# Optimization experiments

Measured on AMD Instinct MI355X. Metric: run time of the kernel, lower is better.

Reference implementation:

```python
import jax, jax.numpy as jnp
import numpy as np

MAX_LEN = 4096
HEAD_DIM = 128
NUM_HEAD = 32
NUM_KV_GROUPS = 8
NUM_HEAD_KV = NUM_HEAD // NUM_KV_GROUPS
BASE = 10000.0


def _rope_tables(seq_len):
    pos = jnp.arange(seq_len, dtype=jnp.float32)
    freq = BASE ** (-(jnp.arange(0, HEAD_DIM, 2, dtype=jnp.float32) / HEAD_DIM))
    ang = pos[:, None] * freq[None, :]  # [n, d/2]
    return jnp.cos(ang), jnp.sin(ang)


def _apply_rope(x, cos, sin):
    # x: [..., n, d]; interleaved even/odd rotation as in the torch RoPe
    even = x[..., ::2]
    odd = x[..., 1::2]
    even_r = even * cos - odd * sin
    odd_r = odd * cos + even * sin
    return jnp.stack([even_r, odd_r], axis=-1).reshape(x.shape)


def setup_inputs() -> dict:
    key = jax.random.key(0)
    ks = jax.random.split(key, 9)
    B, N, D = 4, 1024, NUM_HEAD * HEAD_DIM
    KV = NUM_HEAD_KV * HEAD_DIM
    s = 0.02
    return {
        "x": jax.random.normal(ks[0], (B, N, D), jnp.float32),
        "Wq": jax.random.normal(ks[1], (D, D), jnp.float32) * s,
        "bq": jax.random.normal(ks[2], (D,), jnp.float32) * s,
        "Wk": jax.random.normal(ks[3], (D, KV), jnp.float32) * s,
        "bk": jax.random.normal(ks[4], (KV,), jnp.float32) * s,
        "Wv": jax.random.normal(ks[5], (D, KV), jnp.float32) * s,
        "bv": jax.random.normal(ks[6], (KV,), jnp.float32) * s,
        "Wo": jax.random.normal(ks[7], (D, D), jnp.float32) * s,
        "bo": jax.random.normal(ks[8], (D,), jnp.float32) * s,
    }


def reference(x, Wq, bq, Wk, bk, Wv, bv, Wo, bo):
    B, N, _ = x.shape
    g, h, d = NUM_KV_GROUPS, NUM_HEAD_KV, HEAD_DIM
    scale = d ** (-0.5)

    q = x @ Wq + bq                      # [B, N, g*h*d]
    k = x @ Wk + bk                      # [B, N, h*d]
    v = x @ Wv + bv

    # b n (g h d) -> b g h n d (group-major, matching einops pattern)
    q = q.reshape(B, N, g, h, d).transpose(0, 2, 3, 1, 4)
    k = k.reshape(B, N, h, d).transpose(0, 2, 1, 3)   # b h n d
    v = v.reshape(B, N, h, d).transpose(0, 2, 1, 3)

    cos, sin = _rope_tables(N)
    q = _apply_rope(q, cos, sin)
    k = _apply_rope(k, cos, sin)

    attn = jnp.einsum('bghid,bhjd->bghij', q * scale, k)
    causal = jnp.tril(jnp.ones((N, N), dtype=bool))
    attn = jnp.where(causal, attn, -jnp.inf)
    attn = jax.nn.softmax(attn, axis=-1)

    out = jnp.einsum('bghij,bhjd->bghid', attn, v)
    out = out.transpose(0, 3, 1, 2, 4).reshape(B, N, g * h * d)  # b g h n d -> b n (g h d)
    return out @ Wo + bo
```

## Files before the change

kernel.cpp:

```cpp
#include <hip/hip_runtime.h>
#include <cstdint>
#include <cstddef>

typedef unsigned short u16;
typedef unsigned int u32;

typedef __bf16 bf16x8 __attribute__((ext_vector_type(8)));
typedef float f32x4 __attribute__((ext_vector_type(4)));
typedef u16 u16x8 __attribute__((ext_vector_type(8)));

__device__ __forceinline__ u16 f2bf(float f) {
  union { float f; u32 u; } v; v.f = f;
  u32 r = v.u + 0x7fffu + ((v.u >> 16) & 1u);
  return (u16)(r >> 16);
}
__device__ __forceinline__ float bf2f(u16 h) {
  union { u32 u; float f; } v; v.u = ((u32)h) << 16;
  return v.f;
}

__device__ __forceinline__ void gld16(const u16* g, u16* l) {
  __builtin_amdgcn_global_load_lds((const __attribute__((address_space(1))) u32*)g,
                                   (__attribute__((address_space(3))) u32*)l,
                                   16, 0, 0);
}

template<bool OUT_F32>
__global__ __launch_bounds__(256)
void gemm_bt(const u16* __restrict__ A, const u16* __restrict__ Bt,
             const float* __restrict__ bias, void* __restrict__ C,
             int M, int N, int K) {
  __shared__ __attribute__((aligned(16))) u16 As[2][128*32];
  __shared__ __attribute__((aligned(16))) u16 Bs[2][128*32];
  const int tid  = threadIdx.x;
  const int lane = tid & 63;
  const int wave = tid >> 6;
  const int wm = wave >> 1, wn = wave & 1;
  const int bn = blockIdx.x * 128;
  const int bm = blockIdx.y * 128;
  const int kq = lane >> 4, ml = lane & 15;

  const u16* agp[2]; const u16* bgp[2]; int ldst[2];
#pragma unroll
  for (int j = 0; j < 2; ++j) {
    int s = wave*128 + j*64 + lane;
    int r = s >> 2;
    int c = (s & 3) ^ ((r >> 1) & 3);
    agp[j] = A  + (size_t)(bm + r)*K + c*8;
    bgp[j] = Bt + (size_t)(bn + r)*K + c*8;
    ldst[j] = (wave*128 + j*64)*8;
  }

  auto stage = [&](int p, int k0) {
#pragma unroll
    for (int j = 0; j < 2; ++j) {
      gld16(agp[j] + k0, &As[p][0] + ldst[j]);
      gld16(bgp[j] + k0, &Bs[p][0] + ldst[j]);
    }
  };

  f32x4 acc[4][4] = {};

  auto compute = [&](int p) {
    bf16x8 af[4], bfr[4];
#pragma unroll
    for (int t = 0; t < 4; ++t) {
      int ra = wm*64 + t*16 + ml;
      af[t]  = *(const bf16x8*)(&As[p][0] + (size_t)(ra*4 + (kq ^ ((ra >> 1) & 3)))*8);
      int rb = wn*64 + t*16 + ml;
      bfr[t] = *(const bf16x8*)(&Bs[p][0] + (size_t)(rb*4 + (kq ^ ((rb >> 1) & 3)))*8);
    }
#pragma unroll
    for (int i = 0; i < 4; ++i)
#pragma unroll
      for (int j = 0; j < 4; ++j)
        acc[i][j] = __builtin_amdgcn_mfma_f32_16x16x32_bf16(af[i], bfr[j], acc[i][j], 0, 0, 0);
  };

  stage(0, 0);
  for (int k0 = 0; k0 < K; k0 += 64) {
    __syncthreads();
    if (k0 + 32 < K) stage(1, k0 + 32);
    compute(0);
    __syncthreads();
    if (k0 + 64 < K) stage(0, k0 + 64);
    compute(1);
  }

#pragma unroll
  for (int i = 0; i < 4; ++i) {
    int rg0 = bm + wm*64 + i*16 + kq*4;
#pragma unroll
    for (int j = 0; j < 4; ++j) {
      int cg = bn + wn*64 + j*16 + ml;
      float bv = bias[cg];
#pragma unroll
      for (int r = 0; r < 4; ++r) {
        float v = acc[i][j][r] + bv;
        if (OUT_F32) ((float*)C)[(size_t)(rg0 + r)*N + cg] = v;
        else         ((u16*)C)[(size_t)(rg0 + r)*N + cg]   = f2bf(v);
      }
    }
  }
}

__global__ __launch_bounds__(256)
void attn(const u16* __restrict__ Q, const u16* __restrict__ K,
          const u16* __restrict__ V, u16* __restrict__ ctx) {
  __shared__ __attribute__((aligned(16))) u16 Qs[64*128];
  __shared__ __attribute__((aligned(16))) u16 Ks[64*128];
  __shared__ __attribute__((aligned(16))) u16 Vs[128*64];
  __shared__ __attribute__((aligned(16))) u16 Ps[4][16*72];
  const int qt  = (int)gridDim.x - 1 - (int)blockIdx.x;
  const int bh  = blockIdx.y;
  const int b   = bh >> 5;
  const int kvh = bh & 3;
  const int tid = threadIdx.x;
  const int lane = tid & 63;
  const int wave = tid >> 6;
  const int kq = lane >> 4, ml = lane & 15;

  const u16* Qg = Q + ((size_t)bh*1024 + qt*64)*128;
  const u16* Kg = K + ((size_t)(b*4 + kvh))*1024*128;
  const u16* Vg = V + ((size_t)(b*4 + kvh))*128*1024;

#pragma unroll
  for (int j = 0; j < 4; ++j) {
    int s = wave*256 + j*64 + lane;
    int r = s >> 4, c = (s & 15) ^ (r & 7);
    gld16(Qg + (size_t)r*128 + c*8, Qs + (size_t)(wave*256 + j*64)*8);
  }

  f32x4 o[8] = {};
  float m_i[4] = {-1e30f, -1e30f, -1e30f, -1e30f};
  float l_i[4] = {0.f, 0.f, 0.f, 0.f};

  for (int kt = 0; kt <= qt; ++kt) {
    __syncthreads();
#pragma unroll
    for (int j = 0; j < 4; ++j) {
      int s = wave*256 + j*64 + lane;
      int r = s >> 4, c = (s & 15) ^ (r & 7);
      gld16(Kg + ((size_t)(kt*64 + r))*128 + c*8, Ks + (size_t)(wave*256 + j*64)*8);
    }
#pragma unroll
    for (int j = 0; j < 4; ++j) {
      int s = wave*256 + j*64 + lane;
      int d = s >> 3, c = (s & 7) ^ (d & 7);
      gld16(Vg + (size_t)d*1024 + kt*64 + c*8, Vs + (size_t)(wave*256 + j*64)*8);
    }
    __syncthreads();

    f32x4 sf[4] = {};
#pragma unroll
    for (int ks = 0; ks < 4; ++ks) {
      int rq = wave*16 + ml;
      int cq = ks*4 + kq;
      bf16x8 aq = *(const bf16x8*)(Qs + (size_t)(rq*16 + (cq ^ (rq & 7)))*8);
#pragma unroll
      for (int nt = 0; nt < 4; ++nt) {
        int rk = nt*16 + ml;
        bf16x8 bk = *(const bf16x8*)(Ks + (size_t)(rk*16 + (cq ^ (rk & 7)))*8);
        sf[nt] = __builtin_amdgcn_mfma_f32_16x16x32_bf16(aq, bk, sf[nt], 0, 0, 0);
      }
    }

    const int i0 = qt*64 + wave*16 + kq*4;
    if (kt == qt) {
#pragma unroll
      for (int nt = 0; nt < 4; ++nt) {
        int jg = kt*64 + nt*16 + ml;
#pragma unroll
        for (int r = 0; r < 4; ++r)
          if (jg > i0 + r) sf[nt][r] = -1e30f;
      }
    }
    float rmax[4] = {-1e30f, -1e30f, -1e30f, -1e30f};
#pragma unroll
    for (int nt = 0; nt < 4; ++nt)
#pragma unroll
      for (int r = 0; r < 4; ++r)
        rmax[r] = fmaxf(rmax[r], sf[nt][r]);
#pragma unroll
    for (int r = 0; r < 4; ++r) {
      float v = rmax[r];
      v = fmaxf(v, __shfl_xor(v, 1));
      v = fmaxf(v, __shfl_xor(v, 2));
      v = fmaxf(v, __shfl_xor(v, 4));
      v = fmaxf(v, __shfl_xor(v, 8));
      float mo = m_i[r];
      float mn = fmaxf(mo, v);
      m_i[r] = mn;
      rmax[r] = exp2f(mo - mn);
    }
    float rsum[4] = {0.f, 0.f, 0.f, 0.f};
#pragma unroll
    for (int nt = 0; nt < 4; ++nt)
#pragma unroll
      for (int r = 0; r < 4; ++r) {
        float p = exp2f(sf[nt][r] - m_i[r]);
        rsum[r] += p;
        Ps[wave][(kq*4 + r)*72 + nt*16 + ml] = f2bf(p);
      }
#pragma unroll
    for (int r = 0; r < 4; ++r) {
      float v = rsum[r];
      v += __shfl_xor(v, 1);
      v += __shfl_xor(v, 2);
      v += __shfl_xor(v, 4);
      v += __shfl_xor(v, 8);
      l_i[r] = l_i[r]*rmax[r] + v;
    }
#pragma unroll
    for (int dt = 0; dt < 8; ++dt)
#pragma unroll
      for (int r = 0; r < 4; ++r)
        o[dt][r] *= rmax[r];
    __syncthreads();

#pragma unroll
    for (int ks = 0; ks < 2; ++ks) {
      bf16x8 ap = *(const bf16x8*)(&Ps[wave][ml*72 + ks*32 + kq*8]);
#pragma unroll
      for (int dt = 0; dt < 8; ++dt) {
        int dv = dt*16 + ml;
        int cv = ks*4 + kq;
        bf16x8 bv = *(const bf16x8*)(Vs + (size_t)(dv*8 + (cv ^ (dv & 7)))*8);
        o[dt] = __builtin_amdgcn_mfma_f32_16x16x32_bf16(ap, bv, o[dt], 0, 0, 0);
      }
    }
  }

  const int head = bh & 31;
  float inv[4];
#pragma unroll
  for (int r = 0; r < 4; ++r) inv[r] = 1.f / l_i[r];
  size_t row0 = (size_t)b*1024 + qt*64 + wave*16 + kq*4;
#pragma unroll
  for (int dt = 0; dt < 8; ++dt) {
    int cg = head*128 + dt*16 + ml;
#pragma unroll
    for (int r = 0; r < 4; ++r)
      ctx[(row0 + r)*4096 + cg] = f2bf(o[dt][r]*inv[r]);
  }
}

__global__ void castx(const float* __restrict__ x, u16* __restrict__ xb) {
  size_t i = ((size_t)blockIdx.x*256 + threadIdx.x)*4;
  float4 v = *(const float4*)(x + i);
  ushort4 o; o.x = f2bf(v.x); o.y = f2bf(v.y); o.z = f2bf(v.z); o.w = f2bf(v.w);
  *(ushort4*)(xb + i) = o;
}

__global__ void wtrans(const float* __restrict__ W, u16* __restrict__ Wt, int K, int N) {
  __shared__ u16 t[64*71 + 8];
  const int n0 = blockIdx.x*64, k0 = blockIdx.y*64;
  const int tid = threadIdx.x;
  const int kr = tid >> 4, nc = (tid & 15)*4;
#pragma unroll
  for (int i = 0; i < 4; ++i) {
    float4 v = *(const float4*)(W + (size_t)(k0 + kr + i*16)*N + n0 + nc);
    u16* d = &t[(kr + i*16)*71 + nc];
    d[0] = f2bf(v.x); d[1] = f2bf(v.y); d[2] = f2bf(v.z); d[3] = f2bf(v.w);
  }
  __syncthreads();
  const int n = tid >> 2, k16 = (tid & 3)*16;
  u16x8 lo, hi;
#pragma unroll
  for (int j = 0; j < 8; ++j) lo[j] = t[(k16 + j)*71 + n];
#pragma unroll
  for (int j = 0; j < 8; ++j) hi[j] = t[(k16 + 8 + j)*71 + n];
  u16* dst = Wt + (size_t)(n0 + n)*K + k0 + k16;
  *(u16x8*)(dst)     = lo;
  *(u16x8*)(dst + 8) = hi;
}

__global__ void packbias(const float* __restrict__ bq, const float* __restrict__ bk,
                         const float* __restrict__ bv, float* __restrict__ out) {
  int i = blockIdx.x*256 + threadIdx.x;
  float v;
  if (i < 4096)      v = bq[i];
  else if (i < 4608) v = bk[i - 4096];
  else               v = bv[i - 4608];
  out[i] = v;
}

__global__ void rope_q(const u16* __restrict__ qkv, u16* __restrict__ qr) {
  int idx = blockIdx.x*256 + threadIdx.x;
  int dp = idx & 63;
  int head = (idx >> 6) & 31;
  int n = (idx >> 11) & 1023;
  int b = idx >> 21;
  const u16* src = qkv + ((size_t)(b*1024 + n))*5120 + head*128 + dp*2;
  float e = bf2f(src[0]), od = bf2f(src[1]);
  float freq = exp2f((float)dp * -0.2076205059f);
  float ang = (float)n * freq;
  float c = cosf(ang), s = sinf(ang);
  const float QS = 0.12751747f;
  u16* dst = qr + (((size_t)(b*32 + head))*1024 + n)*128 + dp*2;
  dst[0] = f2bf((e*c - od*s)*QS);
  dst[1] = f2bf((od*c + e*s)*QS);
}

__global__ void rope_k(const u16* __restrict__ qkv, u16* __restrict__ kr) {
  int idx = blockIdx.x*256 + threadIdx.x;
  int dp = idx & 63;
  int kvh = (idx >> 6) & 3;
  int n = (idx >> 8) & 1023;
  int b = idx >> 18;
  const u16* src = qkv + ((size_t)(b*1024 + n))*5120 + 4096 + kvh*128 + dp*2;
  float e = bf2f(src[0]), od = bf2f(src[1]);
  float freq = exp2f((float)dp * -0.2076205059f);
  float ang = (float)n * freq;
  float c = cosf(ang), s = sinf(ang);
  u16* dst = kr + (((size_t)(b*4 + kvh))*1024 + n)*128 + dp*2;
  dst[0] = f2bf(e*c - od*s);
  dst[1] = f2bf(od*c + e*s);
}

__global__ void vtrans(const u16* __restrict__ qkv, u16* __restrict__ vt) {
  __shared__ u16 t[32][40];
  const int nt = blockIdx.x, dt = blockIdx.y, bk = blockIdx.z;
  const int b = bk >> 2, kvh = bk & 3;
  const int tid = threadIdx.x;
  const int r = tid >> 3, c4 = (tid & 7)*4;
  const u16* src = qkv + ((size_t)(b*1024 + nt*32 + r))*5120 + 4608 + kvh*128 + dt*32 + c4;
#pragma unroll
  for (int i = 0; i < 4; ++i) t[r][c4 + i] = src[i];
  __syncthreads();
  u16* dst = vt + ((size_t)((b*4 + kvh)*128 + dt*32 + r))*1024 + nt*32 + c4;
#pragma unroll
  for (int i = 0; i < 4; ++i) dst[i] = t[c4 + i][r];
}

extern "C" void kernel_launch(void* const* d_in, const int* in_sizes, int n_in,
                              void* d_out, int out_size, void* d_ws, size_t ws_size,
                              hipStream_t stream) {
  const float* x  = (const float*)d_in[0];
  const float* Wq = (const float*)d_in[1];
  const float* bq = (const float*)d_in[2];
  const float* Wk = (const float*)d_in[3];
  const float* bk = (const float*)d_in[4];
  const float* Wv = (const float*)d_in[5];
  const float* bv = (const float*)d_in[6];
  const float* Wo = (const float*)d_in[7];
  const float* bo = (const float*)d_in[8];
  float* out = (float*)d_out;

  char* ws = (char*)d_ws;
  u16*   xb   = (u16*)(ws + 0);
  u16*   wqkv = (u16*)(ws + 33554432);
  u16*   wo_t = (u16*)(ws + 75497472);
  float* bqkv = (float*)(ws + 109051904);
  u16*   qkvl = (u16*)(ws + 109072384);
  u16*   qr   = (u16*)(ws + 33554432);
  u16*   kr   = (u16*)(ws + 67108864);
  u16*   vt   = (u16*)(ws + 71303168);
  u16*   ctx  = (u16*)(ws + 0);

  castx<<<16384, 256, 0, stream>>>(x, xb);
  wtrans<<<dim3(64,64), 256, 0, stream>>>(Wq, wqkv, 4096, 4096);
  wtrans<<<dim3(8,64),  256, 0, stream>>>(Wk, wqkv + (size_t)4096*4096, 4096, 512);
  wtrans<<<dim3(8,64),  256, 0, stream>>>(Wv, wqkv + (size_t)4608*4096, 4096, 512);
  wtrans<<<dim3(64,64), 256, 0, stream>>>(Wo, wo_t, 4096, 4096);
  packbias<<<20, 256, 0, stream>>>(bq, bk, bv, bqkv);

  gemm_bt<false><<<dim3(40,32), 256, 0, stream>>>(xb, wqkv, bqkv, qkvl, 4096, 5120, 4096);

  rope_q<<<32768, 256, 0, stream>>>(qkvl, qr);
  rope_k<<<4096,  256, 0, stream>>>(qkvl, kr);
  vtrans<<<dim3(32,4,16), 256, 0, stream>>>(qkvl, vt);

  attn<<<dim3(16,128), 256, 0, stream>>>(qr, kr, vt, ctx);

  gemm_bt<true><<<dim3(32,32), 256, 0, stream>>>(ctx, wo_t, bo, out, 4096, 4096, 4096);
}
```

Before: 832.2 us.

## Replace 128x128 GEMM with 256x256-tile 512-thread pipelined GEMM with XCD remap

Both projection GEMMs move to a new kernel with 256x256 output tiles, 8 waves, BK=64 and a deeper double-buffered pipeline using explicit vmcnt waits and barriers. Workgroup IDs are remapped so that neighbouring tiles land on the same XCD for L2 reuse, and s_setprio raises priority around the MFMA bursts. The larger tiles raise arithmetic intensity and cut global traffic per FLOP. In exchange the kernel uses 128KB of LDS and more registers per wave, and with fewer workgroups (320 and 256) the waves may not fill all CUs evenly.

New measurement: 1.285 ms. +54.4%, slower.

```diff
diff --git a/kernel.cpp b/kernel.cpp
--- a/kernel.cpp
+++ b/kernel.cpp
@@ -26,79 +26,116 @@
 }
 
 template<bool OUT_F32>
-__global__ __launch_bounds__(256)
-void gemm_bt(const u16* __restrict__ A, const u16* __restrict__ Bt,
+__global__ __launch_bounds__(512, 2)
+void gemm256(const u16* __restrict__ A, const u16* __restrict__ Bt,
              const float* __restrict__ bias, void* __restrict__ C,
              int M, int N, int K) {
-  __shared__ __attribute__((aligned(16))) u16 As[2][128*32];
-  __shared__ __attribute__((aligned(16))) u16 Bs[2][128*32];
+  __shared__ __attribute__((aligned(16))) u16 smem[4*16384];
+  u16* const As0 = smem;
+  u16* const Bs0 = smem + 16384;
+  u16* const As1 = smem + 32768;
+  u16* const Bs1 = smem + 49152;
+
   const int tid  = threadIdx.x;
   const int lane = tid & 63;
   const int wave = tid >> 6;
-  const int wm = wave >> 1, wn = wave & 1;
-  const int bn = blockIdx.x * 128;
-  const int bm = blockIdx.y * 128;
+  const int wm = wave >> 2, wn = wave & 3;
   const int kq = lane >> 4, ml = lane & 15;
 
-  const u16* agp[2]; const u16* bgp[2]; int ldst[2];
-#pragma unroll
-  for (int j = 0; j < 2; ++j) {
-    int s = wave*128 + j*64 + lane;
-    int r = s >> 2;
-    int c = (s & 3) ^ ((r >> 1) & 3);
-    agp[j] = A  + (size_t)(bm + r)*K + c*8;
-    bgp[j] = Bt + (size_t)(bn + r)*K + c*8;
-    ldst[j] = (wave*128 + j*64)*8;
-  }
-
-  auto stage = [&](int p, int k0) {
-#pragma unroll
-    for (int j = 0; j < 2; ++j) {
-      gld16(agp[j] + k0, &As[p][0] + ldst[j]);
-      gld16(bgp[j] + k0, &Bs[p][0] + ldst[j]);
-    }
+  const int gx  = gridDim.x;
+  const int nwg = gx * gridDim.y;
+  int lid = blockIdx.y * gx + blockIdx.x;
+  {
+    int q = nwg >> 3, r = nwg & 7;
+    int xcd = lid & 7, loc = lid >> 3;
+    lid = (xcd < r ? xcd * (q + 1) : r * (q + 1) + (xcd - r) * q) + loc;
+  }
+  const int bm = (lid / gx) * 256;
+  const int bn = (lid % gx) * 256;
+
+  const int nt = K >> 6;
+
+  const int rr = tid >> 3;
+  const int cc = (tid & 7) ^ (rr & 7);
+  const u16* const Ag = A  + (size_t)(bm + rr) * K + cc * 8;
+  const u16* const Bg = Bt + (size_t)(bn + rr) * K + cc * 8;
+
+  auto stage = [&](u16* Ad, u16* Bd, int t) {
+    const size_t ko = (size_t)t * 64;
+#pragma unroll
+    for (int j = 0; j < 4; ++j)
+      gld16(Ag + (size_t)j * 64 * K + ko, Ad + ((j * 512 + wave * 64) << 3));
+#pragma unroll
+    for (int j = 0; j < 4; ++j)
+      gld16(Bg + (size_t)j * 64 * K + ko, Bd + ((j * 512 + wave * 64) << 3));
   };
 
-  f32x4 acc[4][4] = {};
-
-  auto compute = [&](int p) {
-    bf16x8 af[4], bfr[4];
-#pragma unroll
-    for (int t = 0; t < 4; ++t) {
-      int ra = wm*64 + t*16 + ml;
-      af[t]  = *(const bf16x8*)(&As[p][0] + (size_t)(ra*4 + (kq ^ ((ra >> 1) & 3)))*8);
-      int rb = wn*64 + t*16 + ml;
-      bfr[t] = *(const bf16x8*)(&Bs[p][0] + (size_t)(rb*4 + (kq ^ ((rb >> 1) & 3)))*8);
-    }
-#pragma unroll
-    for (int i = 0; i < 4; ++i)
-#pragma unroll
-      for (int j = 0; j < 4; ++j)
-        acc[i][j] = __builtin_amdgcn_mfma_f32_16x16x32_bf16(af[i], bfr[j], acc[i][j], 0, 0, 0);
+  f32x4 acc[8][4] = {};
+
+  auto tile = [&](u16* __restrict__ Ab, u16* __restrict__ Bb, int t) {
+    bf16x8 a0[8], b0[4];
+#pragma unroll
+    for (int mi = 0; mi < 8; ++mi) {
+      int ra = wm * 128 + mi * 16 + ml;
+      a0[mi] = *(const bf16x8*)(Ab + (size_t)(ra * 8 + (kq ^ (ra & 7))) * 8);
+    }
+#pragma unroll
+    for (int ni = 0; ni < 4; ++ni) {
+      int rb = wn * 64 + ni * 16 + ml;
+      b0[ni] = *(const bf16x8*)(Bb + (size_t)(rb * 8 + (kq ^ (rb & 7))) * 8);
+    }
+    __builtin_amdgcn_s_setprio(1);
+#pragma unroll
+    for (int mi = 0; mi < 8; ++mi)
+#pragma unroll
+      for (int ni = 0; ni < 4; ++ni)
+        acc[mi][ni] = __builtin_amdgcn_mfma_f32_16x16x32_bf16(a0[mi], b0[ni], acc[mi][ni], 0, 0, 0);
+    __builtin_amdgcn_s_setprio(0);
+#pragma unroll
+    for (int mi = 0; mi < 8; ++mi) {
+      int ra = wm * 128 + mi * 16 + ml;
+      a0[mi] = *(const bf16x8*)(Ab + (size_t)(ra * 8 + ((4 + kq) ^ (ra & 7))) * 8);
+    }
+#pragma unroll
+    for (int ni = 0; ni < 4; ++ni) {
+      int rb = wn * 64 + ni * 16 + ml;
+      b0[ni] = *(const bf16x8*)(Bb + (size_t)(rb * 8 + ((4 + kq) ^ (rb & 7))) * 8);
+    }
+    asm volatile("s_waitcnt lgkmcnt(0)\n\ts_barrier" ::: "memory");
+    if (t + 2 < nt) stage(Ab, Bb, t + 2);
+    __builtin_amdgcn_s_setprio(1);
+#pragma unroll
+    for (int mi = 0; mi < 8; ++mi)
+#pragma unroll
+      for (int ni = 0; ni < 4; ++ni)
+        acc[mi][ni] = __builtin_amdgcn_mfma_f32_16x16x32_bf16(a0[mi], b0[ni], acc[mi][ni], 0, 0, 0);
+    __builtin_amdgcn_s_setprio(0);
+    if (t + 2 < nt)      asm volatile("s_waitcnt vmcnt(8)\n\ts_barrier" ::: "memory");
+    else if (t + 1 < nt) asm volatile("s_waitcnt vmcnt(0)\n\ts_barrier" ::: "memory");
+    else                 asm volatile("s_barrier" ::: "memory");
   };
 
-  stage(0, 0);
-  for (int k0 = 0; k0 < K; k0 += 64) {
-    __syncthreads();
-    if (k0 + 32 < K) stage(1, k0 + 32);
-    compute(0);
-    __syncthreads();
-    if (k0 + 64 < K) stage(0, k0 + 64);
-    compute(1);
-  }
-
-#pragma unroll
-  for (int i = 0; i < 4; ++i) {
-    int rg0 = bm + wm*64 + i*16 + kq*4;
-#pragma unroll
-    for (int j = 0; j < 4; ++j) {
-      int cg = bn + wn*64 + j*16 + ml;
+  stage(As0, Bs0, 0);
+  stage(As1, Bs1, 1);
+  asm volatile("s_waitcnt vmcnt(8)\n\ts_barrier" ::: "memory");
+
+  for (int t = 0; t < nt; t += 2) {
+    tile(As0, Bs0, t);
+    tile(As1, Bs1, t + 1);
+  }
+
+#pragma unroll
+  for (int mi = 0; mi < 8; ++mi) {
+    int rg0 = bm + wm * 128 + mi * 16 + kq * 4;
+#pragma unroll
+    for (int ni = 0; ni < 4; ++ni) {
+      int cg = bn + wn * 64 + ni * 16 + ml;
       float bv = bias[cg];
 #pragma unroll
       for (int r = 0; r < 4; ++r) {
-        float v = acc[i][j][r] + bv;
-        if (OUT_F32) ((float*)C)[(size_t)(rg0 + r)*N + cg] = v;
-        else         ((u16*)C)[(size_t)(rg0 + r)*N + cg]   = f2bf(v);
+        float v = acc[mi][ni][r] + bv;
+        if (OUT_F32) ((float*)C)[(size_t)(rg0 + r) * N + cg] = v;
+        else         ((u16*)C)[(size_t)(rg0 + r) * N + cg]   = f2bf(v);
       }
     }
   }
@@ -365,7 +402,7 @@
   wtrans<<<dim3(64,64), 256, 0, stream>>>(Wo, wo_t, 4096, 4096);
   packbias<<<20, 256, 0, stream>>>(bq, bk, bv, bqkv);
 
-  gemm_bt<false><<<dim3(40,32), 256, 0, stream>>>(xb, wqkv, bqkv, qkvl, 4096, 5120, 4096);
+  gemm256<false><<<dim3(20,16), 512, 0, stream>>>(xb, wqkv, bqkv, qkvl, 4096, 5120, 4096);
 
   rope_q<<<32768, 256, 0, stream>>>(qkvl, qr);
   rope_k<<<4096,  256, 0, stream>>>(qkvl, kr);
@@ -373,5 +410,5 @@
 
   attn<<<dim3(16,128), 256, 0, stream>>>(qr, kr, vt, ctx);
 
-  gemm_bt<true><<<dim3(32,32), 256, 0, stream>>>(ctx, wo_t, bo, out, 4096, 4096, 4096);
-}
+  gemm256<true><<<dim3(16,16), 512, 0, stream>>>(ctx, wo_t, bo, out, 4096, 4096, 4096);
+}
```

## Double-buffer V tile and overlap previous P·V MFMA with next tile loads

Applied to the files above, without the earlier changes.

The attention loop now keeps two LDS buffers for the V tile. Each iteration issues the async K/V loads for tile kt first, then computes the P·V product of the previous tile from the other buffer while those loads are in flight. A final P·V step runs after the loop, and one __syncthreads per iteration is dropped. The cost is 16KB of extra LDS per block, which may limit how many blocks fit on a CU.

Result: no change. 831.3 us (-0.1%).

```diff
diff --git a/kernel.cpp b/kernel.cpp
--- a/kernel.cpp
+++ b/kernel.cpp
@@ -109,7 +109,7 @@
           const u16* __restrict__ V, u16* __restrict__ ctx) {
   __shared__ __attribute__((aligned(16))) u16 Qs[64*128];
   __shared__ __attribute__((aligned(16))) u16 Ks[64*128];
-  __shared__ __attribute__((aligned(16))) u16 Vs[128*64];
+  __shared__ __attribute__((aligned(16))) u16 Vs[2][128*64];
   __shared__ __attribute__((aligned(16))) u16 Ps[4][16*72];
   const int qt  = (int)gridDim.x - 1 - (int)blockIdx.x;
   const int bh  = blockIdx.y;
@@ -136,6 +136,7 @@
   float l_i[4] = {0.f, 0.f, 0.f, 0.f};
 
   for (int kt = 0; kt <= qt; ++kt) {
+    const int p = kt & 1;
     __syncthreads();
 #pragma unroll
     for (int j = 0; j < 4; ++j) {
@@ -147,7 +148,21 @@
     for (int j = 0; j < 4; ++j) {
       int s = wave*256 + j*64 + lane;
       int d = s >> 3, c = (s & 7) ^ (d & 7);
-      gld16(Vg + (size_t)d*1024 + kt*64 + c*8, Vs + (size_t)(wave*256 + j*64)*8);
+      gld16(Vg + (size_t)d*1024 + kt*64 + c*8, &Vs[p][0] + (size_t)(wave*256 + j*64)*8);
+    }
+
+    if (kt > 0) {
+#pragma unroll
+      for (int ks = 0; ks < 2; ++ks) {
+        bf16x8 ap = *(const bf16x8*)(&Ps[wave][ml*72 + ks*32 + kq*8]);
+#pragma unroll
+        for (int dt = 0; dt < 8; ++dt) {
+          int dv = dt*16 + ml;
+          int cv = ks*4 + kq;
+          bf16x8 bv = *(const bf16x8*)(&Vs[p^1][0] + (size_t)(dv*8 + (cv ^ (dv & 7)))*8);
+          o[dt] = __builtin_amdgcn_mfma_f32_16x16x32_bf16(ap, bv, o[dt], 0, 0, 0);
+        }
+      }
     }
     __syncthreads();
 
@@ -198,9 +213,9 @@
     for (int nt = 0; nt < 4; ++nt)
 #pragma unroll
       for (int r = 0; r < 4; ++r) {
-        float p = exp2f(sf[nt][r] - m_i[r]);
-        rsum[r] += p;
-        Ps[wave][(kq*4 + r)*72 + nt*16 + ml] = f2bf(p);
+        float p2 = exp2f(sf[nt][r] - m_i[r]);
+        rsum[r] += p2;
+        Ps[wave][(kq*4 + r)*72 + nt*16 + ml] = f2bf(p2);
       }
 #pragma unroll
     for (int r = 0; r < 4; ++r) {
@@ -216,8 +231,10 @@
 #pragma unroll
       for (int r = 0; r < 4; ++r)
         o[dt][r] *= rmax[r];
-    __syncthreads();
-
+  }
+
+  {
+    const int p = qt & 1;
 #pragma unroll
     for (int ks = 0; ks < 2; ++ks) {
       bf16x8 ap = *(const bf16x8*)(&Ps[wave][ml*72 + ks*32 + kq*8]);
@@ -225,7 +242,7 @@
       for (int dt = 0; dt < 8; ++dt) {
         int dv = dt*16 + ml;
         int cv = ks*4 + kq;
-        bf16x8 bv = *(const bf16x8*)(Vs + (size_t)(dv*8 + (cv ^ (dv & 7)))*8);
+        bf16x8 bv = *(const bf16x8*)(&Vs[p][0] + (size_t)(dv*8 + (cv ^ (dv & 7)))*8);
         o[dt] = __builtin_amdgcn_mfma_f32_16x16x32_bf16(ap, bv, o[dt], 0, 0, 0);
       }
     }
```
